# Kernel tuning notes

Measured on AMD Instinct MI355X. Metric: run time of the kernel, lower is better.

The kernel has to match this reference:

```python
import jax, jax.numpy as jnp
import numpy as np

P_THRESHOLD = 0.6
K_CAP = 16


def softmax_m1(x):
    # f(x) = (exp(x)-1) / sum(exp(x)-1), as in the torch module
    fx = jnp.expm1(x)
    return fx / fx.sum(-1, keepdims=True)


def align_chars(start_map, nb_map, max_ch):
    # eval-mode recurrence of NeighborDecoder.align_chars, run for a fixed
    # max_ch steps (no data-dependent early break; char_masks carry the
    # finished state exactly as in torch).
    b = start_map.shape[0]

    def step(carry, i):
        char_map, finished = carry  # [b, N+1], [b] int32
        mask = (finished == 0).astype(char_map.dtype)
        out = (char_map, mask)  # emitted BEFORE the update, matching torch
        finished = finished + (char_map[:, -1] > P_THRESHOLD).astype(jnp.int32)
        kk = jnp.minimum(1 + 2 * i, K_CAP).astype(char_map.dtype)
        cmd = softmax_m1(jax.lax.stop_gradient(char_map) * kk)  # .detach() in torch
        nxt = jnp.einsum('bn,bnm->bm', cmd, nb_map)
        return (nxt, finished), out

    init = (start_map, jnp.zeros(b, jnp.int32))
    _, (maps, masks) = jax.lax.scan(step, init, jnp.arange(max_ch))
    return maps.transpose(1, 0, 2), masks.T  # [b, T, N+1], [b, T]


def setup_inputs() -> dict:
    key = jax.random.key(0)
    ks = jax.random.split(key, 8)
    b, c, h, w = 32, 384, 16, 64
    num_classes = 97
    s = 1.0 / np.sqrt(c)
    return {
        'x': jax.random.normal(ks[0], (b, c, h, w), jnp.float32),
        'eos_emb': (jax.random.normal(ks[1], (c,), jnp.float32) * 0.02),
        'q_w': jax.random.normal(ks[2], (c, c), jnp.float32) * s,
        'q_b': jnp.zeros((c,), jnp.float32),
        'k_w': jax.random.normal(ks[3], (c, c), jnp.float32) * s,
        'k_b': jnp.zeros((c,), jnp.float32),
        'nav_w': jax.random.normal(ks[4], (1, c, c), jnp.float32) * 0.01,
        'nav_b': jnp.zeros((1,), jnp.float32),
        'cls_w': jax.random.normal(ks[5], (num_classes, c), jnp.float32) * s,
        'cls_b': jnp.zeros((num_classes,), jnp.float32),
        'max_char': 48,
    }


def reference(x, eos_emb, q_w, q_b, k_w, k_b, nav_w, nav_b, cls_w, cls_b, max_char):
    b, c, h, w = x.shape
    scale = float(c) ** 0.5
    xt = x.reshape(b, c, h * w).transpose(0, 2, 1)  # [b, N, c]
    g = xt.mean(axis=1)  # [b, c]
    x_ext = jnp.concatenate(
        [xt, jnp.broadcast_to(eos_emb, (b, 1, c))], axis=1)  # [b, N+1, c]

    q_start = g @ q_w.T + q_b                      # [b, c]
    k_feat = x_ext @ k_w.T + k_b                   # [b, N+1, c]
    start_map = jnp.einsum('bnc,bc->bn', k_feat, q_start) / scale
    start_map = jax.nn.softmax(start_map, axis=1)  # [b, N+1]

    q_feat = xt @ q_w.T + q_b                      # [b, N, c]
    # BilinearLayer with out=1: einsum('bim,mn,bjn->bij') + bias
    nb_map = jnp.einsum('bim,mn,bjn->bij', q_feat, nav_w[0], k_feat) + nav_b[0]
    nb_map = jax.nn.softmax(nb_map / scale, axis=2)  # [b, N, N+1]

    last = jnp.zeros((h * w + 1,), x.dtype).at[-1].set(1.0)
    nb_map = jnp.concatenate(
        [nb_map, jnp.broadcast_to(last, (b, 1, h * w + 1))], axis=1)  # [b, N+1, N+1]

    char_maps, char_masks = align_chars(start_map, nb_map, max_char)
    char_feats = jnp.einsum('btn,bnc->btc', char_maps, x_ext)
    char_feats = char_feats * char_masks[..., None]
    logits = char_feats @ cls_w.T + cls_b          # [b, T, num_classes]
    return logits, char_feats, char_maps, char_masks, nb_map
```

## Files before the change

### kernel.cpp

```cpp
#include <hip/hip_runtime.h>
#include <cstdint>
#include <cstddef>

#define BB   32
#define CC   384
#define NN   1024
#define N1   1025
#define TT   48
#define NCLS 97
#define NBL_LD 1088
#define NBTS   1056

static constexpr float INV_SCALE = 1.0f / 19.595917942265423f;

using bf16x8 = __attribute__((ext_vector_type(8))) __bf16;
using f32x4  = __attribute__((ext_vector_type(4))) float;

static constexpr size_t OFF_LOGITS = 0;
static constexpr size_t OFF_CFEAT  = 148992;
static constexpr size_t OFF_CMAPS  = 738816;
static constexpr size_t OFF_CMASK  = 2313216;
static constexpr size_t OFF_NB     = 2314752;

static constexpr size_t OFF_XB     = 0;
static constexpr size_t OFF_WGEM   = 25165824;
static constexpr size_t OFF_BIAS   = 25755648;
static constexpr size_t OFF_G      = 25758720;
static constexpr size_t OFF_QSTART = 25807872;
static constexpr size_t OFF_KEOS   = 25857024;
static constexpr size_t OFF_STATS  = 25858560;
static constexpr size_t OFF_MAPSBF = 26120704;
static constexpr size_t OFF_CMD    = 29266432;
static constexpr size_t OFF_PSUM   = 29536768;
static constexpr size_t OFF_XBT    = 29569536;
static constexpr size_t OFF_NBL    = 29569536;
static constexpr size_t OFF_OUT    = 100942336;
static constexpr size_t OFF_NBT    = 100942336;

__device__ __forceinline__ float bf2f(uint u) {
    union { uint i; float f; } v; v.i = u << 16; return v.f;
}
__device__ __forceinline__ ushort f2bf(float f) {
    union { float f; uint i; } v; v.f = f;
    uint r = v.i + 0x7fffu + ((v.i >> 16) & 1u);
    return (ushort)(r >> 16);
}

__global__ __launch_bounds__(256) void k_conv_mean(
    const float* __restrict__ x, ushort* __restrict__ xb, float* __restrict__ g)
{
    int row  = blockIdx.x * 4 + (threadIdx.x >> 6);
    int lane = threadIdx.x & 63;
    const float* src = x + (size_t)row * NN;
    ushort* dst = xb + (size_t)row * NN;
    float s = 0.f;
#pragma unroll
    for (int q = 0; q < 4; q++) {
        float4 v = ((const float4*)src)[q * 64 + lane];
        s += v.x + v.y + v.z + v.w;
        ushort4 p; p.x = f2bf(v.x); p.y = f2bf(v.y); p.z = f2bf(v.z); p.w = f2bf(v.w);
        ((ushort4*)dst)[q * 64 + lane] = p;
    }
#pragma unroll
    for (int o = 32; o; o >>= 1) s += __shfl_down(s, o);
    if (lane == 0) g[row] = s * (1.0f / NN);
}

__global__ __launch_bounds__(256) void k_transpose(
    const ushort* __restrict__ xb, ushort* __restrict__ xbT)
{
    int b = blockIdx.z, c0 = blockIdx.x * 64, n0 = blockIdx.y * 64;
    __shared__ ushort t[64][65];
    int ur = threadIdx.x >> 5, uc = threadIdx.x & 31;
    const ushort* src = xb + ((size_t)b * CC + c0) * NN + n0;
#pragma unroll
    for (int p = 0; p < 8; p++) {
        int c = p * 8 + ur;
        uint v = ((const uint*)(src + (size_t)c * NN))[uc];
        t[c][uc * 2]     = (ushort)(v & 0xffffu);
        t[c][uc * 2 + 1] = (ushort)(v >> 16);
    }
    __syncthreads();
    ushort* dst = xbT + ((size_t)b * N1 + n0) * CC + c0;
#pragma unroll
    for (int p = 0; p < 8; p++) {
        int n = p * 8 + ur;
        uint v = (uint)t[uc * 2][n] | (((uint)t[uc * 2 + 1][n]) << 16);
        ((uint*)(dst + (size_t)n * CC))[uc] = v;
    }
}

__global__ void k_eosrow(const float* __restrict__ eos, ushort* __restrict__ xbT)
{
    int c = threadIdx.x;
    xbT[((size_t)blockIdx.x * N1 + NN) * CC + c] = f2bf(eos[c]);
}

__global__ void k_wk(const float* __restrict__ k_w, const float* __restrict__ k_b,
                     ushort* __restrict__ Wgem, float* __restrict__ bias)
{
    int j = blockIdx.x, c = threadIdx.x;
    Wgem[(size_t)j * CC + c] = f2bf(k_w[(size_t)j * CC + c]);
    if (c == 0) bias[j] = k_b[j];
}

__global__ void k_w2(const float* __restrict__ nav_w, const float* __restrict__ q_w,
                     const float* __restrict__ q_b, ushort* __restrict__ Wgem,
                     float* __restrict__ bias)
{
    int m = blockIdx.x, c = threadIdx.x;
    float acc = 0.f, accb = 0.f;
    for (int k = 0; k < CC; k++) {
        float nv = nav_w[(size_t)k * CC + m];
        acc  += nv * q_w[(size_t)k * CC + c];
        accb += nv * q_b[k];
    }
    Wgem[(size_t)(CC + m) * CC + c] = f2bf(acc);
    if (c == 0) bias[CC + m] = accb;
}

__global__ void k_qstart(const float* __restrict__ g, const float* __restrict__ q_w,
                         const float* __restrict__ q_b, float* __restrict__ q_start)
{
    int b = blockIdx.x, k = threadIdx.x;
    __shared__ float gs[CC];
    gs[k] = g[(size_t)b * CC + k];
    __syncthreads();
    float acc = q_b[k];
    const float* w = q_w + (size_t)k * CC;
    for (int c = 0; c < CC; c++) acc += gs[c] * w[c];
    q_start[(size_t)b * CC + k] = acc;
}

__global__ void k_keos(const float* __restrict__ eos, const float* __restrict__ k_w,
                       const float* __restrict__ k_b, float* __restrict__ keos,
                       ushort* __restrict__ Out)
{
    int co = threadIdx.x;
    float acc = k_b[co];
    const float* w = k_w + (size_t)co * CC;
    for (int c = 0; c < CC; c++) acc += eos[c] * w[c];
    keos[co] = acc;
    ushort v = f2bf(acc);
    for (int b = 0; b < BB; b++) Out[((size_t)b * N1 + NN) * 768 + co] = v;
}

template<int MODE, int NTN, int PERB>
__global__ __launch_bounds__(256) void k_gemm(
    const ushort* __restrict__ Aall, size_t strideAb, int lda,
    const ushort* __restrict__ Ball, size_t strideBb, int ldb,
    ushort* __restrict__ Cout, size_t strideCb, int ldc,
    const float* __restrict__ bias)
{
    int wid = blockIdx.x;
    int xcd = wid & 7;
    int work = xcd * (PERB * 4) + (wid >> 3);
    int b = work / PERB;
    int r = work - b * PERB;
    int m0 = (r / NTN) * 128, n0 = (r % NTN) * 128;

    const ushort* A  = Aall + (size_t)b * strideAb;
    const ushort* Bp = Ball + (size_t)b * strideBb;
    __shared__ ushort sbuf[16384];
    ushort* As = sbuf;
    ushort* Bs = sbuf + 8192;
    int tid = threadIdx.x, wave = tid >> 6, lane = tid & 63;
    int wm = wave >> 1, wn = wave & 1;
    f32x4 acc[4][4] = {};

    uint4 ra[4], rb[4];
    auto load_tiles = [&](int k0) {
#pragma unroll
        for (int q = 0; q < 4; q++) {
            int idx = q * 256 + tid, rr = idx >> 3, c8 = (idx & 7) * 8;
            ra[q] = *(const uint4*)(A  + (size_t)(m0 + rr) * lda + k0 + c8);
            rb[q] = *(const uint4*)(Bp + (size_t)(n0 + rr) * ldb + k0 + c8);
        }
    };
    load_tiles(0);
    for (int k0 = 0; k0 < CC; k0 += 64) {
        __syncthreads();
#pragma unroll
        for (int q = 0; q < 4; q++) {
            int idx = q * 256 + tid, rr = idx >> 3, c8 = (idx & 7) * 8;
            *(uint4*)(As + rr * 64 + c8) = ra[q];
            *(uint4*)(Bs + rr * 64 + c8) = rb[q];
        }
        __syncthreads();
        if (k0 + 64 < CC) load_tiles(k0 + 64);
#pragma unroll
        for (int h = 0; h < 2; h++) {
            bf16x8 af[4], bfr[4];
#pragma unroll
            for (int i = 0; i < 4; i++) {
                int row = wm * 64 + i * 16 + (lane & 15);
                af[i]  = *(const bf16x8*)(As + row * 64 + h * 32 + (lane >> 4) * 8);
                int col = wn * 64 + i * 16 + (lane & 15);
                bfr[i] = *(const bf16x8*)(Bs + col * 64 + h * 32 + (lane >> 4) * 8);
            }
#pragma unroll
            for (int i = 0; i < 4; i++)
#pragma unroll
                for (int j = 0; j < 4; j++)
                    acc[i][j] = __builtin_amdgcn_mfma_f32_16x16x32_bf16(af[i], bfr[j], acc[i][j], 0, 0, 0);
        }
    }
    __syncthreads();
#pragma unroll
    for (int i = 0; i < 4; i++) {
        int rl = wm * 64 + i * 16 + ((lane >> 4) << 2);
#pragma unroll
        for (int j = 0; j < 4; j++) {
            int cl = wn * 64 + j * 16 + (lane & 15);
            float bv = (MODE == 0) ? bias[n0 + cl] : 0.f;
#pragma unroll
            for (int rr = 0; rr < 4; rr++) {
                float val = (MODE == 0) ? (acc[i][j][rr] + bv) : (acc[i][j][rr] * INV_SCALE);
                sbuf[(rl + rr) * 128 + cl] = f2bf(val);
            }
        }
    }
    __syncthreads();
    ushort* Cb = Cout + (size_t)b * strideCb;
#pragma unroll
    for (int q = 0; q < 8; q++) {
        int idx = q * 256 + tid, row = idx >> 4, seg = idx & 15;
        *(uint4*)(Cb + (size_t)(m0 + row) * ldc + n0 + seg * 8) =
            *(const uint4*)(sbuf + row * 128 + seg * 8);
    }
}

__global__ __launch_bounds__(1024) void k_start(
    const ushort* __restrict__ Out, const float* __restrict__ q_start,
    float* __restrict__ cmaps)
{
    int b = blockIdx.x, tid = threadIdx.x;
    __shared__ float qs[CC];
    __shared__ float red[16];
    __shared__ float bc;
    if (tid < CC) qs[tid] = q_start[(size_t)b * CC + tid];
    __syncthreads();
    auto dot = [&](int n) {
        const uint4* row = (const uint4*)(Out + ((size_t)b * N1 + n) * 768);
        float acc = 0.f;
        for (int c8 = 0; c8 < CC / 8; c8++) {
            uint4 u = row[c8];
            const ushort* us = (const ushort*)&u;
#pragma unroll
            for (int e = 0; e < 8; e++) acc += bf2f(us[e]) * qs[c8 * 8 + e];
        }
        return acc * INV_SCALE;
    };
    float v0 = dot(tid);
    float v1 = (tid == 0) ? dot(1024) : -1e30f;
    float lm = fmaxf(v0, v1);
#pragma unroll
    for (int o = 32; o; o >>= 1) lm = fmaxf(lm, __shfl_down(lm, o));
    if ((tid & 63) == 0) red[tid >> 6] = lm;
    __syncthreads();
    if (tid == 0) { float m = red[0]; for (int i = 1; i < 16; i++) m = fmaxf(m, red[i]); bc = m; }
    __syncthreads();
    float bmax = bc;
    float e0 = __expf(v0 - bmax);
    float e1 = (tid == 0) ? __expf(v1 - bmax) : 0.f;
    float ls = e0 + e1;
#pragma unroll
    for (int o = 32; o; o >>= 1) ls += __shfl_down(ls, o);
    if ((tid & 63) == 0) red[tid >> 6] = ls;
    __syncthreads();
    if (tid == 0) { float s = 0.f; for (int i = 0; i < 16; i++) s += red[i]; bc = s; }
    __syncthreads();
    float inv = 1.f / bc;
    float* o = cmaps + ((size_t)b * TT) * N1;
    o[tid] = e0 * inv;
    if (tid == 0) o[1024] = e1 * inv;
}

__global__ __launch_bounds__(256) void k_eoscol_nbl(
    const ushort* __restrict__ Out, const float* __restrict__ keos, ushort* __restrict__ nbL)
{
    int gw = blockIdx.x * 4 + (threadIdx.x >> 6);
    int lane = threadIdx.x & 63;
    for (int rr = 0; rr < 4; rr++) {
        int gi = gw * 4 + rr, b = gi >> 10, i = gi & 1023;
        const ushort* row = Out + ((size_t)b * N1 + i) * 768 + 384;
        float acc = 0.f;
        for (int c = lane; c < CC; c += 64) acc += bf2f(row[c]) * keos[c];
#pragma unroll
        for (int o = 32; o; o >>= 1) acc += __shfl_down(acc, o);
        if (lane == 0) nbL[((size_t)b * N1 + i) * NBL_LD + 1024] = f2bf(acc * INV_SCALE);
    }
}

__global__ __launch_bounds__(256) void k_softnb2(
    const ushort* __restrict__ nbL, float* __restrict__ nb, float2* __restrict__ stats)
{
    int bi = blockIdx.x;
    int b = bi >> 10, i = bi & 1023;
    const ushort* row = nbL + ((size_t)b * N1 + i) * NBL_LD;
    int tid = threadIdx.x;
    uint2 u = *(const uint2*)(row + tid * 4);
    float v0 = bf2f(u.x & 0xffffu), v1 = bf2f(u.x >> 16);
    float v2 = bf2f(u.y & 0xffffu), v3 = bf2f(u.y >> 16);
    float vt = (tid == 0) ? bf2f(row[1024]) : -1e30f;
    __shared__ float r1[4]; __shared__ float bc;
    float lm = fmaxf(fmaxf(fmaxf(v0, v1), fmaxf(v2, v3)), vt);
#pragma unroll
    for (int o = 32; o; o >>= 1) lm = fmaxf(lm, __shfl_down(lm, o));
    if ((tid & 63) == 0) r1[tid >> 6] = lm;
    __syncthreads();
    if (tid == 0) bc = fmaxf(fmaxf(r1[0], r1[1]), fmaxf(r1[2], r1[3]));
    __syncthreads();
    float m = bc;
    float e0 = __expf(v0 - m), e1 = __expf(v1 - m), e2 = __expf(v2 - m), e3 = __expf(v3 - m);
    float et = (tid == 0) ? __expf(vt - m) : 0.f;
    float s = e0 + e1 + e2 + e3 + et;
#pragma unroll
    for (int o = 32; o; o >>= 1) s += __shfl_down(s, o);
    if ((tid & 63) == 0) r1[tid >> 6] = s;
    __syncthreads();
    if (tid == 0) bc = r1[0] + r1[1] + r1[2] + r1[3];
    __syncthreads();
    float inv = 1.f / bc;
    float* orow = nb + ((size_t)b * N1 + i) * N1;
    orow[tid * 4 + 0] = e0 * inv;
    orow[tid * 4 + 1] = e1 * inv;
    orow[tid * 4 + 2] = e2 * inv;
    orow[tid * 4 + 3] = e3 * inv;
    if (tid == 0) { orow[1024] = et * inv; stats[b * 1024 + i] = make_float2(m, inv); }
}

__global__ void k_onehot2(float* __restrict__ nb, ushort* __restrict__ nbT)
{
    int b = blockIdx.x;
    float* row = nb + ((size_t)b * N1 + NN) * N1;
    for (int j = threadIdx.x; j < N1; j += 256) {
        row[j] = (j == 1024) ? 1.f : 0.f;
        nbT[((size_t)b * N1 + j) * NBTS + 1024] = (j == 1024) ? (ushort)0x3F80 : (ushort)0;
    }
}

__global__ __launch_bounds__(256) void k_transq(
    const ushort* __restrict__ nbL, const float2* __restrict__ stats,
    ushort* __restrict__ nbT)
{
    int b = blockIdx.z, n0 = blockIdx.x * 64, j0 = blockIdx.y * 64;
    __shared__ ushort tile[64][80];
    __shared__ float2 st[64];
    int tid = threadIdx.x;
    if (tid < 64) st[tid] = stats[b * 1024 + n0 + tid];
    __syncthreads();
#pragma unroll
    for (int q = 0; q < 2; q++) {
        int idx = q * 256 + tid, rl = idx >> 3, ch = idx & 7;
        const ushort* src = nbL + ((size_t)b * N1 + n0 + rl) * NBL_LD + j0 + ch * 8;
        uint4 u = *(const uint4*)src;
        float2 s = st[rl];
        const ushort* us = (const ushort*)&u;
#pragma unroll
        for (int k = 0; k < 8; k++)
            tile[ch * 8 + k][rl] = f2bf(__expf(bf2f(us[k]) - s.x) * s.y);
    }
    __syncthreads();
#pragma unroll
    for (int q = 0; q < 2; q++) {
        int idx = q * 256 + tid, jl = idx >> 3, seg = idx & 7;
        int j = j0 + jl;
        if (j <= 1024) {
            uint4 v = *(const uint4*)&tile[jl][seg * 8];
            *(uint4*)(nbT + ((size_t)b * N1 + j) * NBTS + n0 + seg * 8) = v;
        }
    }
}

__global__ __launch_bounds__(256) void k_cmd0(
    const float* __restrict__ cmaps, float* __restrict__ cmd_out, float* __restrict__ ps_out)
{
    int b = blockIdx.x, tid = threadIdx.x;
    __shared__ float red[4];
    const float* m = cmaps + (size_t)b * TT * N1;
    float s = 0.f;
    for (int n = tid; n < N1; n += 256) {
        float c = expm1f(m[n]);
        cmd_out[(size_t)b * 1056 + n] = c;
        s += c;
    }
#pragma unroll
    for (int o = 32; o; o >>= 1) s += __shfl_down(s, o);
    if ((tid & 63) == 0) red[tid >> 6] = s;
    __syncthreads();
    if (tid == 0) ps_out[b * 128] = red[0] + red[1] + red[2] + red[3];
    else if (tid < 128) ps_out[b * 128 + tid] = 0.f;
}

__global__ __launch_bounds__(256) void k_step2(
    float* __restrict__ cmaps, const ushort* __restrict__ nbT,
    const float* __restrict__ cmd_in, float* __restrict__ cmd_out,
    const float* __restrict__ ps_in, float* __restrict__ ps_out, int t)
{
    int b = blockIdx.y, blk = blockIdx.x, j0 = blk * 16;
    int tid = threadIdx.x, wave = tid >> 6, lane = tid & 63;
    const ushort* base = nbT + (size_t)b * N1 * NBTS;
    uint4 rv[4][2]; ushort tl[4];
#pragma unroll
    for (int r = 0; r < 4; r++) {
        int j = j0 + wave * 4 + r; if (j > 1024) j = 1024;
        const ushort* row = base + (size_t)j * NBTS;
        rv[r][0] = *(const uint4*)(row + lane * 8);
        rv[r][1] = *(const uint4*)(row + 512 + lane * 8);
        tl[r] = row[1024];
    }
    __shared__ __align__(16) float cmd[1028];
    __shared__ float red[8];
    const float* ci = cmd_in + (size_t)b * 1056;
    *(float4*)(cmd + tid * 4) = *(const float4*)(ci + tid * 4);
    if (tid == 0) cmd[1024] = ci[1024];
    float pv = (tid < 65) ? ps_in[b * 128 + tid] : 0.f;
#pragma unroll
    for (int o = 32; o; o >>= 1) pv += __shfl_down(pv, o);
    if (lane == 0) red[wave] = pv;
    __syncthreads();
    float inv = 1.f / (red[0] + red[1] + red[2] + red[3]);
    int kkn = 3 + 2 * t; if (kkn > 16) kkn = 16;
    float kknf = (float)kkn;
    float cns = 0.f;
#pragma unroll
    for (int r = 0; r < 4; r++) {
        const ushort* p0 = (const ushort*)&rv[r][0];
        const ushort* p1 = (const ushort*)&rv[r][1];
        int n0 = lane * 8;
        float acc = 0.f;
#pragma unroll
        for (int e = 0; e < 8; e++) acc += bf2f(p0[e]) * cmd[n0 + e];
#pragma unroll
        for (int e = 0; e < 8; e++) acc += bf2f(p1[e]) * cmd[512 + n0 + e];
#pragma unroll
        for (int o = 32; o; o >>= 1) acc += __shfl_down(acc, o);
        int j = j0 + wave * 4 + r;
        if (lane == 0 && j <= 1024) {
            acc += cmd[1024] * bf2f(tl[r]);
            float mo = acc * inv;
            cmaps[((size_t)b * TT + t + 1) * N1 + j] = mo;
            float cn = expm1f(kknf * mo);
            cmd_out[(size_t)b * 1056 + j] = cn;
            cns += cn;
        }
    }
    if (lane == 0) red[4 + wave] = cns;
    __syncthreads();
    if (tid == 0) ps_out[b * 128 + blk] = red[4] + red[5] + red[6] + red[7];
}

__global__ void k_masks(const float* __restrict__ cmaps, float* __restrict__ cmask)
{
    int b = threadIdx.x;
    if (b < BB) {
        int fin = 0;
        for (int t = 0; t < TT; t++) {
            cmask[b * TT + t] = (fin == 0) ? 1.f : 0.f;
            fin += (cmaps[((size_t)b * TT + t) * N1 + 1024] > 0.6f) ? 1 : 0;
        }
    }
}

__global__ void k_mapsbf(const float* __restrict__ cmaps, ushort* __restrict__ mb)
{
    size_t i = (size_t)blockIdx.x * 256 + threadIdx.x;
    size_t bt = i >> 10; int n = (int)(i & 1023);
    mb[i] = f2bf(cmaps[bt * N1 + n]);
}

__global__ __launch_bounds__(256) void k_cfeat(
    const ushort* __restrict__ mapsbf, const ushort* __restrict__ xb,
    const float* __restrict__ cmaps, const float* __restrict__ eos,
    const float* __restrict__ masks, float* __restrict__ cfeat)
{
    int b = blockIdx.x;
    int wave = threadIdx.x >> 6, lane = threadIdx.x & 63;
    f32x4 acc[3][6] = {};
    const ushort* Ab = mapsbf + (size_t)b * TT * 1024;
    const ushort* Bb = xb + (size_t)b * CC * NN;
    for (int k0 = 0; k0 < NN; k0 += 32) {
        int kk_ = k0 + (lane >> 4) * 8;
        bf16x8 af[3], bfr[6];
#pragma unroll
        for (int i = 0; i < 3; i++)
            af[i] = *(const bf16x8*)(Ab + (size_t)(i * 16 + (lane & 15)) * 1024 + kk_);
#pragma unroll
        for (int j = 0; j < 6; j++)
            bfr[j] = *(const bf16x8*)(Bb + (size_t)(wave * 96 + j * 16 + (lane & 15)) * NN + kk_);
#pragma unroll
        for (int i = 0; i < 3; i++)
#pragma unroll
            for (int j = 0; j < 6; j++)
                acc[i][j] = __builtin_amdgcn_mfma_f32_16x16x32_bf16(af[i], bfr[j], acc[i][j], 0, 0, 0);
    }
#pragma unroll
    for (int i = 0; i < 3; i++) {
        int tbase = i * 16 + ((lane >> 4) << 2);
#pragma unroll
        for (int j = 0; j < 6; j++) {
            int c = wave * 96 + j * 16 + (lane & 15);
            float ev = eos[c];
#pragma unroll
            for (int rr = 0; rr < 4; rr++) {
                int tt = tbase + rr;
                float mlast = cmaps[((size_t)b * TT + tt) * N1 + 1024];
                float val = (acc[i][j][rr] + mlast * ev) * masks[b * TT + tt];
                cfeat[((size_t)b * TT + tt) * CC + c] = val;
            }
        }
    }
}

__global__ __launch_bounds__(128) void k_logits(
    const float* __restrict__ cfeat, const float* __restrict__ cls_w,
    const float* __restrict__ cls_b, float* __restrict__ out)
{
    int bt = blockIdx.x;
    __shared__ float row[CC];
    for (int c = threadIdx.x; c < CC; c += 128) row[c] = cfeat[(size_t)bt * CC + c];
    __syncthreads();
    int j = threadIdx.x;
    if (j < NCLS) {
        float acc = cls_b[j];
        const float* w = cls_w + (size_t)j * CC;
        for (int c = 0; c < CC; c++) acc += row[c] * w[c];
        out[(size_t)bt * NCLS + j] = acc;
    }
}

extern "C" void kernel_launch(void* const* d_in, const int* in_sizes, int n_in,
                              void* d_out, int out_size, void* d_ws, size_t ws_size,
                              hipStream_t stream)
{
    (void)in_sizes; (void)n_in; (void)out_size; (void)ws_size;
    const float* x     = (const float*)d_in[0];
    const float* eos   = (const float*)d_in[1];
    const float* q_w   = (const float*)d_in[2];
    const float* q_b   = (const float*)d_in[3];
    const float* k_w   = (const float*)d_in[4];
    const float* k_b   = (const float*)d_in[5];
    const float* nav_w = (const float*)d_in[6];
    const float* cls_w = (const float*)d_in[8];
    const float* cls_b = (const float*)d_in[9];

    char* ws = (char*)d_ws;
    ushort* xb     = (ushort*)(ws + OFF_XB);
    ushort* Wgem   = (ushort*)(ws + OFF_WGEM);
    float*  bias   = (float*)(ws + OFF_BIAS);
    float*  g      = (float*)(ws + OFF_G);
    float*  qstart = (float*)(ws + OFF_QSTART);
    float*  keos   = (float*)(ws + OFF_KEOS);
    float2* stats  = (float2*)(ws + OFF_STATS);
    ushort* mapsbf = (ushort*)(ws + OFF_MAPSBF);
    float*  cmdbuf = (float*)(ws + OFF_CMD);
    float*  psbuf  = (float*)(ws + OFF_PSUM);
    ushort* xbT    = (ushort*)(ws + OFF_XBT);
    ushort* nbL    = (ushort*)(ws + OFF_NBL);
    ushort* Out    = (ushort*)(ws + OFF_OUT);
    ushort* nbT    = (ushort*)(ws + OFF_NBT);

    float* out     = (float*)d_out;
    float* logits  = out + OFF_LOGITS;
    float* cfeat   = out + OFF_CFEAT;
    float* cmaps   = out + OFF_CMAPS;
    float* cmask   = out + OFF_CMASK;
    float* nb      = out + OFF_NB;

    k_conv_mean<<<3072, 256, 0, stream>>>(x, xb, g);
    k_transpose<<<dim3(6, 16, BB), 256, 0, stream>>>(xb, xbT);
    k_eosrow<<<BB, CC, 0, stream>>>(eos, xbT);
    k_wk<<<CC, CC, 0, stream>>>(k_w, k_b, Wgem, bias);
    k_w2<<<CC, CC, 0, stream>>>(nav_w, q_w, q_b, Wgem, bias);
    k_qstart<<<BB, CC, 0, stream>>>(g, q_w, q_b, qstart);
    k_keos<<<1, CC, 0, stream>>>(eos, k_w, k_b, keos, Out);

    k_gemm<0, 6, 48><<<1536, 256, 0, stream>>>(
        xbT, (size_t)N1 * CC, CC, Wgem, 0, CC, Out, (size_t)N1 * 768, 768, bias);

    k_start<<<BB, 1024, 0, stream>>>(Out, qstart, cmaps);
    k_cmd0<<<BB, 256, 0, stream>>>(cmaps, cmdbuf, psbuf);
    k_eoscol_nbl<<<2048, 256, 0, stream>>>(Out, keos, nbL);

    k_gemm<1, 8, 64><<<2048, 256, 0, stream>>>(
        Out + 384, (size_t)N1 * 768, 768, Out, (size_t)N1 * 768, 768,
        nbL, (size_t)N1 * NBL_LD, NBL_LD, nullptr);

    k_softnb2<<<BB * NN, 256, 0, stream>>>(nbL, nb, stats);
    k_onehot2<<<BB, 256, 0, stream>>>(nb, nbT);
    k_transq<<<dim3(16, 17, BB), 256, 0, stream>>>(nbL, stats, nbT);

    for (int t = 0; t < TT - 1; t++)
        k_step2<<<dim3(65, BB), 256, 0, stream>>>(
            cmaps, nbT,
            cmdbuf + (size_t)(t & 1) * 33792, cmdbuf + (size_t)((t + 1) & 1) * 33792,
            psbuf + (size_t)(t & 1) * 4096,  psbuf + (size_t)((t + 1) & 1) * 4096, t);

    k_masks<<<1, 64, 0, stream>>>(cmaps, cmask);
    k_mapsbf<<<6144, 256, 0, stream>>>(cmaps, mapsbf);
    k_cfeat<<<BB, 256, 0, stream>>>(mapsbf, xb, cmaps, eos, cmask, cfeat);
    k_logits<<<BB * TT, 128, 0, stream>>>(cfeat, cls_w, cls_b, logits);
}
```

Measured before the change: 1.165 ms.

## Fuse recurrence steps into one persistent kernel with per-batch spin barriers

Replaces the 47 per-step recurrence launches with a single persistent kernel of 256 blocks, eight per batch, that loops over all steps. Blocks sync through an atomic counter per batch and exchange char maps through global memory. Each block recomputes the expm1 and softmax normaliser itself, and row loads are double-buffered. The change also XOR-swizzles the GEMM shared-memory tiles to avoid bank conflicts and vectorises the softmax row store; the risks are spin-barrier deadlock if blocks are not all co-resident, and the extra redundant expm1 work per block.

```diff
diff --git a/kernel.cpp b/kernel.cpp
--- a/kernel.cpp
+++ b/kernel.cpp
@@ -30,8 +30,7 @@
 static constexpr size_t OFF_KEOS   = 25857024;
 static constexpr size_t OFF_STATS  = 25858560;
 static constexpr size_t OFF_MAPSBF = 26120704;
-static constexpr size_t OFF_CMD    = 29266432;
-static constexpr size_t OFF_PSUM   = 29536768;
+static constexpr size_t OFF_BAR    = 29266432;
 static constexpr size_t OFF_XBT    = 29569536;
 static constexpr size_t OFF_NBL    = 29569536;
 static constexpr size_t OFF_OUT    = 100942336;
@@ -182,21 +181,23 @@
         __syncthreads();
 #pragma unroll
         for (int q = 0; q < 4; q++) {
-            int idx = q * 256 + tid, rr = idx >> 3, c8 = (idx & 7) * 8;
-            *(uint4*)(As + rr * 64 + c8) = ra[q];
-            *(uint4*)(Bs + rr * 64 + c8) = rb[q];
+            int idx = q * 256 + tid, rr = idx >> 3, ch = idx & 7;
+            int sw = (ch ^ (rr & 7)) << 3;
+            *(uint4*)(As + rr * 64 + sw) = ra[q];
+            *(uint4*)(Bs + rr * 64 + sw) = rb[q];
         }
         __syncthreads();
         if (k0 + 64 < CC) load_tiles(k0 + 64);
 #pragma unroll
         for (int h = 0; h < 2; h++) {
             bf16x8 af[4], bfr[4];
+            int chb = h * 4 + (lane >> 4);
 #pragma unroll
             for (int i = 0; i < 4; i++) {
                 int row = wm * 64 + i * 16 + (lane & 15);
-                af[i]  = *(const bf16x8*)(As + row * 64 + h * 32 + (lane >> 4) * 8);
+                af[i]  = *(const bf16x8*)(As + row * 64 + ((chb ^ (row & 7)) << 3));
                 int col = wn * 64 + i * 16 + (lane & 15);
-                bfr[i] = *(const bf16x8*)(Bs + col * 64 + h * 32 + (lane >> 4) * 8);
+                bfr[i] = *(const bf16x8*)(Bs + col * 64 + ((chb ^ (col & 7)) << 3));
             }
 #pragma unroll
             for (int i = 0; i < 4; i++)
@@ -323,21 +324,17 @@
     __syncthreads();
     float inv = 1.f / bc;
     float* orow = nb + ((size_t)b * N1 + i) * N1;
-    orow[tid * 4 + 0] = e0 * inv;
-    orow[tid * 4 + 1] = e1 * inv;
-    orow[tid * 4 + 2] = e2 * inv;
-    orow[tid * 4 + 3] = e3 * inv;
+    float4 ov = make_float4(e0 * inv, e1 * inv, e2 * inv, e3 * inv);
+    *(float4*)(orow + tid * 4) = ov;
     if (tid == 0) { orow[1024] = et * inv; stats[b * 1024 + i] = make_float2(m, inv); }
 }
 
-__global__ void k_onehot2(float* __restrict__ nb, ushort* __restrict__ nbT)
+__global__ void k_onehot(float* __restrict__ nb)
 {
     int b = blockIdx.x;
     float* row = nb + ((size_t)b * N1 + NN) * N1;
-    for (int j = threadIdx.x; j < N1; j += 256) {
+    for (int j = threadIdx.x; j < N1; j += 256)
         row[j] = (j == 1024) ? 1.f : 0.f;
-        nbT[((size_t)b * N1 + j) * NBTS + 1024] = (j == 1024) ? (ushort)0x3F80 : (ushort)0;
-    }
 }
 
 __global__ __launch_bounds__(256) void k_transq(
@@ -373,82 +370,120 @@
     }
 }
 
-__global__ __launch_bounds__(256) void k_cmd0(
-    const float* __restrict__ cmaps, float* __restrict__ cmd_out, float* __restrict__ ps_out)
-{
-    int b = blockIdx.x, tid = threadIdx.x;
-    __shared__ float red[4];
-    const float* m = cmaps + (size_t)b * TT * N1;
-    float s = 0.f;
-    for (int n = tid; n < N1; n += 256) {
-        float c = expm1f(m[n]);
-        cmd_out[(size_t)b * 1056 + n] = c;
-        s += c;
-    }
-#pragma unroll
-    for (int o = 32; o; o >>= 1) s += __shfl_down(s, o);
-    if ((tid & 63) == 0) red[tid >> 6] = s;
-    __syncthreads();
-    if (tid == 0) ps_out[b * 128] = red[0] + red[1] + red[2] + red[3];
-    else if (tid < 128) ps_out[b * 128 + tid] = 0.f;
-}
-
-__global__ __launch_bounds__(256) void k_step2(
-    float* __restrict__ cmaps, const ushort* __restrict__ nbT,
-    const float* __restrict__ cmd_in, float* __restrict__ cmd_out,
-    const float* __restrict__ ps_in, float* __restrict__ ps_out, int t)
-{
-    int b = blockIdx.y, blk = blockIdx.x, j0 = blk * 16;
+__global__ void k_barinit(uint* __restrict__ bar) { bar[threadIdx.x] = 0u; }
+
+__device__ __forceinline__ float dot16(uint4 r0, uint4 r1,
+                                       const float* cA, const float* cB)
+{
+    const ushort* p0 = (const ushort*)&r0;
+    const ushort* p1 = (const ushort*)&r1;
+    float acc = 0.f;
+#pragma unroll
+    for (int e = 0; e < 8; e++) acc += bf2f(p0[e]) * cA[e];
+#pragma unroll
+    for (int e = 0; e < 8; e++) acc += bf2f(p1[e]) * cB[e];
+    return acc;
+}
+
+__global__ __launch_bounds__(512) void k_rec(
+    float* __restrict__ cmaps, const ushort* __restrict__ nbT, uint* __restrict__ bar)
+{
+    int blk = blockIdx.x;
+    int b = blk >> 3, chunk = blk & 7;
     int tid = threadIdx.x, wave = tid >> 6, lane = tid & 63;
+    int j0 = chunk * 128;
     const ushort* base = nbT + (size_t)b * N1 * NBTS;
-    uint4 rv[4][2]; ushort tl[4];
-#pragma unroll
-    for (int r = 0; r < 4; r++) {
-        int j = j0 + wave * 4 + r; if (j > 1024) j = 1024;
-        const ushort* row = base + (size_t)j * NBTS;
-        rv[r][0] = *(const uint4*)(row + lane * 8);
-        rv[r][1] = *(const uint4*)(row + 512 + lane * 8);
-        tl[r] = row[1024];
-    }
     __shared__ __align__(16) float cmd[1028];
     __shared__ float red[8];
-    const float* ci = cmd_in + (size_t)b * 1056;
-    *(float4*)(cmd + tid * 4) = *(const float4*)(ci + tid * 4);
-    if (tid == 0) cmd[1024] = ci[1024];
-    float pv = (tid < 65) ? ps_in[b * 128 + tid] : 0.f;
-#pragma unroll
-    for (int o = 32; o; o >>= 1) pv += __shfl_down(pv, o);
-    if (lane == 0) red[wave] = pv;
-    __syncthreads();
-    float inv = 1.f / (red[0] + red[1] + red[2] + red[3]);
-    int kkn = 3 + 2 * t; if (kkn > 16) kkn = 16;
-    float kknf = (float)kkn;
-    float cns = 0.f;
-#pragma unroll
-    for (int r = 0; r < 4; r++) {
-        const ushort* p0 = (const ushort*)&rv[r][0];
-        const ushort* p1 = (const ushort*)&rv[r][1];
-        int n0 = lane * 8;
-        float acc = 0.f;
-#pragma unroll
-        for (int e = 0; e < 8; e++) acc += bf2f(p0[e]) * cmd[n0 + e];
-#pragma unroll
-        for (int e = 0; e < 8; e++) acc += bf2f(p1[e]) * cmd[512 + n0 + e];
-#pragma unroll
-        for (int o = 32; o; o >>= 1) acc += __shfl_down(acc, o);
-        int j = j0 + wave * 4 + r;
-        if (lane == 0 && j <= 1024) {
-            acc += cmd[1024] * bf2f(tl[r]);
-            float mo = acc * inv;
-            cmaps[((size_t)b * TT + t + 1) * N1 + j] = mo;
-            float cn = expm1f(kknf * mo);
-            cmd_out[(size_t)b * 1056 + j] = cn;
-            cns += cn;
-        }
-    }
-    if (lane == 0) red[4 + wave] = cns;
-    __syncthreads();
-    if (tid == 0) ps_out[b * 128 + blk] = red[4] + red[5] + red[6] + red[7];
+    __shared__ float sinv;
+
+    for (int t = 0; t < TT - 1; ++t) {
+        const float* mrow = cmaps + ((size_t)b * TT + t) * N1;
+        int kki = 1 + 2 * t; if (kki > 16) kki = 16;
+        float kkf = (float)kki;
+        float part = 0.f;
+#pragma unroll
+        for (int q = 0; q < 2; ++q) {
+            int n = q * 512 + tid;
+            float m = __hip_atomic_load(mrow + n, __ATOMIC_RELAXED, __HIP_MEMORY_SCOPE_AGENT);
+            float e = expm1f(kkf * m);
+            cmd[n] = e; part += e;
+        }
+        if (tid == 0) {
+            float m = __hip_atomic_load(mrow + 1024, __ATOMIC_RELAXED, __HIP_MEMORY_SCOPE_AGENT);
+            float e = expm1f(kkf * m);
+            cmd[1024] = e; part += e;
+        }
+#pragma unroll
+        for (int o = 32; o; o >>= 1) part += __shfl_down(part, o);
+        if (lane == 0) red[wave] = part;
+        __syncthreads();
+        if (tid == 0) {
+            float s = 0.f;
+#pragma unroll
+            for (int w = 0; w < 8; w++) s += red[w];
+            sinv = 1.f / s;
+        }
+        __syncthreads();
+        float inv = sinv;
+        float cA[8], cB[8];
+        *(float4*)&cA[0] = *(const float4*)(cmd + lane * 8);
+        *(float4*)&cA[4] = *(const float4*)(cmd + lane * 8 + 4);
+        *(float4*)&cB[0] = *(const float4*)(cmd + 512 + lane * 8);
+        *(float4*)&cB[4] = *(const float4*)(cmd + 512 + lane * 8 + 4);
+        float* orow = cmaps + ((size_t)b * TT + t + 1) * N1;
+        int rbase = j0 + wave * 16;
+
+        uint4 cur[4][2], nxt[4][2];
+#pragma unroll
+        for (int r = 0; r < 4; ++r) {
+            const ushort* row = base + (size_t)(rbase + r) * NBTS;
+            cur[r][0] = *(const uint4*)(row + lane * 8);
+            cur[r][1] = *(const uint4*)(row + 512 + lane * 8);
+        }
+        for (int g = 0; g < 4; ++g) {
+            if (g < 3) {
+#pragma unroll
+                for (int r = 0; r < 4; ++r) {
+                    const ushort* row = base + (size_t)(rbase + (g + 1) * 4 + r) * NBTS;
+                    nxt[r][0] = *(const uint4*)(row + lane * 8);
+                    nxt[r][1] = *(const uint4*)(row + 512 + lane * 8);
+                }
+            }
+#pragma unroll
+            for (int r = 0; r < 4; ++r) {
+                float acc = dot16(cur[r][0], cur[r][1], cA, cB);
+#pragma unroll
+                for (int o = 32; o; o >>= 1) acc += __shfl_down(acc, o);
+                if (lane == 0)
+                    __hip_atomic_store(orow + rbase + g * 4 + r, acc * inv,
+                                       __ATOMIC_RELAXED, __HIP_MEMORY_SCOPE_AGENT);
+            }
+            if (g < 3) {
+#pragma unroll
+                for (int r = 0; r < 4; ++r) { cur[r][0] = nxt[r][0]; cur[r][1] = nxt[r][1]; }
+            }
+        }
+        if (chunk == 7 && wave == 7) {
+            const ushort* row = base + (size_t)1024 * NBTS;
+            uint4 r0 = *(const uint4*)(row + lane * 8);
+            uint4 r1 = *(const uint4*)(row + 512 + lane * 8);
+            float acc = dot16(r0, r1, cA, cB);
+#pragma unroll
+            for (int o = 32; o; o >>= 1) acc += __shfl_down(acc, o);
+            if (lane == 0)
+                __hip_atomic_store(orow + 1024, (acc + cmd[1024]) * inv,
+                                   __ATOMIC_RELAXED, __HIP_MEMORY_SCOPE_AGENT);
+        }
+        __syncthreads();
+        if (tid == 0) {
+            __hip_atomic_fetch_add(&bar[b], 1u, __ATOMIC_RELEASE, __HIP_MEMORY_SCOPE_AGENT);
+            uint want = 8u * (uint)(t + 1);
+            while (__hip_atomic_load(&bar[b], __ATOMIC_ACQUIRE, __HIP_MEMORY_SCOPE_AGENT) < want)
+                __builtin_amdgcn_s_sleep(8);
+        }
+        __syncthreads();
+    }
 }
 
 __global__ void k_masks(const float* __restrict__ cmaps, float* __restrict__ cmask)
@@ -554,8 +589,7 @@
     float*  keos   = (float*)(ws + OFF_KEOS);
     float2* stats  = (float2*)(ws + OFF_STATS);
     ushort* mapsbf = (ushort*)(ws + OFF_MAPSBF);
-    float*  cmdbuf = (float*)(ws + OFF_CMD);
-    float*  psbuf  = (float*)(ws + OFF_PSUM);
+    uint*   bar    = (uint*)(ws + OFF_BAR);
     ushort* xbT    = (ushort*)(ws + OFF_XBT);
     ushort* nbL    = (ushort*)(ws + OFF_NBL);
     ushort* Out    = (ushort*)(ws + OFF_OUT);
@@ -575,12 +609,12 @@
     k_w2<<<CC, CC, 0, stream>>>(nav_w, q_w, q_b, Wgem, bias);
     k_qstart<<<BB, CC, 0, stream>>>(g, q_w, q_b, qstart);
     k_keos<<<1, CC, 0, stream>>>(eos, k_w, k_b, keos, Out);
+    k_barinit<<<1, 32, 0, stream>>>(bar);
 
     k_gemm<0, 6, 48><<<1536, 256, 0, stream>>>(
         xbT, (size_t)N1 * CC, CC, Wgem, 0, CC, Out, (size_t)N1 * 768, 768, bias);
 
     k_start<<<BB, 1024, 0, stream>>>(Out, qstart, cmaps);
-    k_cmd0<<<BB, 256, 0, stream>>>(cmaps, cmdbuf, psbuf);
     k_eoscol_nbl<<<2048, 256, 0, stream>>>(Out, keos, nbL);
 
     k_gemm<1, 8, 64><<<2048, 256, 0, stream>>>(
@@ -588,14 +622,10 @@
         nbL, (size_t)N1 * NBL_LD, NBL_LD, nullptr);
 
     k_softnb2<<<BB * NN, 256, 0, stream>>>(nbL, nb, stats);
-    k_onehot2<<<BB, 256, 0, stream>>>(nb, nbT);
+    k_onehot<<<BB, 256, 0, stream>>>(nb);
     k_transq<<<dim3(16, 17, BB), 256, 0, stream>>>(nbL, stats, nbT);
 
-    for (int t = 0; t < TT - 1; t++)
-        k_step2<<<dim3(65, BB), 256, 0, stream>>>(
-            cmaps, nbT,
-            cmdbuf + (size_t)(t & 1) * 33792, cmdbuf + (size_t)((t + 1) & 1) * 33792,
-            psbuf + (size_t)(t & 1) * 4096,  psbuf + (size_t)((t + 1) & 1) * 4096, t);
+    k_rec<<<256, 512, 0, stream>>>(cmaps, nbT, bar);
 
     k_masks<<<1, 64, 0, stream>>>(cmaps, cmask);
     k_mapsbf<<<6144, 256, 0, stream>>>(cmaps, mapsbf);
```

New measurement: 1.925 ms (median of 5 runs). 65.3% more time.

## Swizzle GEMM LDS tiles, restructure recurrence step to row-per-lane with fewer blocks

Applied to the files above, without the earlier changes.

The GEMM's shared-memory tiles get an XOR swizzle on the 8-element chunk index to reduce LDS bank conflicts on the MFMA fragment reads. The per-step recurrence kernel now gives each lane one output row and each wave a quarter of the reduction dimension. It runs 17 blocks per batch instead of 65, with a software-prefetched register pipeline, and drops the cross-lane shuffle reductions per row. The nbT eos column is no longer written, and the eos term is added only for row 1024. The softmax output store is vectorised to float4. The new step layout has each lane reading a separate row, so memory accesses are strided across lanes and may coalesce worse.

```diff
diff --git a/kernel.cpp b/kernel.cpp
--- a/kernel.cpp
+++ b/kernel.cpp
@@ -182,21 +182,23 @@
         __syncthreads();
 #pragma unroll
         for (int q = 0; q < 4; q++) {
-            int idx = q * 256 + tid, rr = idx >> 3, c8 = (idx & 7) * 8;
-            *(uint4*)(As + rr * 64 + c8) = ra[q];
-            *(uint4*)(Bs + rr * 64 + c8) = rb[q];
+            int idx = q * 256 + tid, rr = idx >> 3, ch = idx & 7;
+            int sw = (ch ^ (rr & 7)) << 3;
+            *(uint4*)(As + rr * 64 + sw) = ra[q];
+            *(uint4*)(Bs + rr * 64 + sw) = rb[q];
         }
         __syncthreads();
         if (k0 + 64 < CC) load_tiles(k0 + 64);
 #pragma unroll
         for (int h = 0; h < 2; h++) {
             bf16x8 af[4], bfr[4];
+            int chb = h * 4 + (lane >> 4);
 #pragma unroll
             for (int i = 0; i < 4; i++) {
                 int row = wm * 64 + i * 16 + (lane & 15);
-                af[i]  = *(const bf16x8*)(As + row * 64 + h * 32 + (lane >> 4) * 8);
+                af[i]  = *(const bf16x8*)(As + row * 64 + ((chb ^ (row & 7)) << 3));
                 int col = wn * 64 + i * 16 + (lane & 15);
-                bfr[i] = *(const bf16x8*)(Bs + col * 64 + h * 32 + (lane >> 4) * 8);
+                bfr[i] = *(const bf16x8*)(Bs + col * 64 + ((chb ^ (col & 7)) << 3));
             }
 #pragma unroll
             for (int i = 0; i < 4; i++)
@@ -323,21 +325,17 @@
     __syncthreads();
     float inv = 1.f / bc;
     float* orow = nb + ((size_t)b * N1 + i) * N1;
-    orow[tid * 4 + 0] = e0 * inv;
-    orow[tid * 4 + 1] = e1 * inv;
-    orow[tid * 4 + 2] = e2 * inv;
-    orow[tid * 4 + 3] = e3 * inv;
+    float4 ov = make_float4(e0 * inv, e1 * inv, e2 * inv, e3 * inv);
+    *(float4*)(orow + tid * 4) = ov;
     if (tid == 0) { orow[1024] = et * inv; stats[b * 1024 + i] = make_float2(m, inv); }
 }
 
-__global__ void k_onehot2(float* __restrict__ nb, ushort* __restrict__ nbT)
+__global__ void k_onehot(float* __restrict__ nb)
 {
     int b = blockIdx.x;
     float* row = nb + ((size_t)b * N1 + NN) * N1;
-    for (int j = threadIdx.x; j < N1; j += 256) {
+    for (int j = threadIdx.x; j < N1; j += 256)
         row[j] = (j == 1024) ? 1.f : 0.f;
-        nbT[((size_t)b * N1 + j) * NBTS + 1024] = (j == 1024) ? (ushort)0x3F80 : (ushort)0;
-    }
 }
 
 __global__ __launch_bounds__(256) void k_transq(
@@ -393,62 +391,76 @@
     else if (tid < 128) ps_out[b * 128 + tid] = 0.f;
 }
 
-__global__ __launch_bounds__(256) void k_step2(
+__global__ __launch_bounds__(256) void k_step3(
     float* __restrict__ cmaps, const ushort* __restrict__ nbT,
     const float* __restrict__ cmd_in, float* __restrict__ cmd_out,
     const float* __restrict__ ps_in, float* __restrict__ ps_out, int t)
 {
-    int b = blockIdx.y, blk = blockIdx.x, j0 = blk * 16;
+    int b = blockIdx.y, blk = blockIdx.x;
     int tid = threadIdx.x, wave = tid >> 6, lane = tid & 63;
-    const ushort* base = nbT + (size_t)b * N1 * NBTS;
-    uint4 rv[4][2]; ushort tl[4];
-#pragma unroll
-    for (int r = 0; r < 4; r++) {
-        int j = j0 + wave * 4 + r; if (j > 1024) j = 1024;
-        const ushort* row = base + (size_t)j * NBTS;
-        rv[r][0] = *(const uint4*)(row + lane * 8);
-        rv[r][1] = *(const uint4*)(row + 512 + lane * 8);
-        tl[r] = row[1024];
-    }
+    int j0 = blk * 64;
+    int rowc = j0 + lane; if (rowc > 1024) rowc = 1024;
+    const ushort* rp = nbT + ((size_t)b * N1 + rowc) * NBTS + wave * 256;
+
+    uint4 buf[8];
+#pragma unroll
+    for (int p = 0; p < 8; ++p) buf[p] = *(const uint4*)(rp + p * 8);
+
     __shared__ __align__(16) float cmd[1028];
-    __shared__ float red[8];
+    __shared__ float partial[4][64];
+    __shared__ float sred;
     const float* ci = cmd_in + (size_t)b * 1056;
     *(float4*)(cmd + tid * 4) = *(const float4*)(ci + tid * 4);
     if (tid == 0) cmd[1024] = ci[1024];
-    float pv = (tid < 65) ? ps_in[b * 128 + tid] : 0.f;
-#pragma unroll
-    for (int o = 32; o; o >>= 1) pv += __shfl_down(pv, o);
-    if (lane == 0) red[wave] = pv;
-    __syncthreads();
-    float inv = 1.f / (red[0] + red[1] + red[2] + red[3]);
-    int kkn = 3 + 2 * t; if (kkn > 16) kkn = 16;
-    float kknf = (float)kkn;
-    float cns = 0.f;
-#pragma unroll
-    for (int r = 0; r < 4; r++) {
-        const ushort* p0 = (const ushort*)&rv[r][0];
-        const ushort* p1 = (const ushort*)&rv[r][1];
-        int n0 = lane * 8;
-        float acc = 0.f;
-#pragma unroll
-        for (int e = 0; e < 8; e++) acc += bf2f(p0[e]) * cmd[n0 + e];
-#pragma unroll
-        for (int e = 0; e < 8; e++) acc += bf2f(p1[e]) * cmd[512 + n0 + e];
-#pragma unroll
-        for (int o = 32; o; o >>= 1) acc += __shfl_down(acc, o);
-        int j = j0 + wave * 4 + r;
-        if (lane == 0 && j <= 1024) {
-            acc += cmd[1024] * bf2f(tl[r]);
-            float mo = acc * inv;
+    if (wave == 0) {
+        float pv = (lane < 17) ? ps_in[b * 128 + lane] : 0.f;
+#pragma unroll
+        for (int o = 16; o; o >>= 1) pv += __shfl_down(pv, o);
+        if (lane == 0) sred = pv;
+    }
+    __syncthreads();
+    float inv = 1.f / sred;
+
+    const float* cq = cmd + wave * 256;
+    float acc = 0.f;
+    for (int g = 0; g < 4; ++g) {
+        uint4 nbuf[8];
+        if (g < 3) {
+#pragma unroll
+            for (int p = 0; p < 8; ++p)
+                nbuf[p] = *(const uint4*)(rp + (g + 1) * 64 + p * 8);
+        }
+#pragma unroll
+        for (int p = 0; p < 8; ++p) {
+            const ushort* u = (const ushort*)&buf[p];
+            const float* cc = cq + g * 64 + p * 8;
+#pragma unroll
+            for (int e = 0; e < 8; ++e) acc += bf2f(u[e]) * cc[e];
+        }
+        if (g < 3) {
+#pragma unroll
+            for (int p = 0; p < 8; ++p) buf[p] = nbuf[p];
+        }
+    }
+    partial[wave][lane] = acc;
+    __syncthreads();
+    if (wave == 0) {
+        int j = j0 + lane;
+        bool valid = (j <= 1024);
+        float s = partial[0][lane] + partial[1][lane] + partial[2][lane] + partial[3][lane];
+        if (j == 1024) s += cmd[1024];
+        float mo = s * inv;
+        int kkn = 3 + 2 * t; if (kkn > 16) kkn = 16;
+        float cn = valid ? expm1f((float)kkn * mo) : 0.f;
+        if (valid) {
             cmaps[((size_t)b * TT + t + 1) * N1 + j] = mo;
-            float cn = expm1f(kknf * mo);
             cmd_out[(size_t)b * 1056 + j] = cn;
-            cns += cn;
-        }
-    }
-    if (lane == 0) red[4 + wave] = cns;
-    __syncthreads();
-    if (tid == 0) ps_out[b * 128 + blk] = red[4] + red[5] + red[6] + red[7];
+        }
+        float ps = cn;
+#pragma unroll
+        for (int o = 32; o; o >>= 1) ps += __shfl_down(ps, o);
+        if (lane == 0) ps_out[b * 128 + blk] = ps;
+    }
 }
 
 __global__ void k_masks(const float* __restrict__ cmaps, float* __restrict__ cmask)
@@ -588,11 +600,11 @@
         nbL, (size_t)N1 * NBL_LD, NBL_LD, nullptr);
 
     k_softnb2<<<BB * NN, 256, 0, stream>>>(nbL, nb, stats);
-    k_onehot2<<<BB, 256, 0, stream>>>(nb, nbT);
+    k_onehot<<<BB, 256, 0, stream>>>(nb);
     k_transq<<<dim3(16, 17, BB), 256, 0, stream>>>(nbL, stats, nbT);
 
     for (int t = 0; t < TT - 1; t++)
-        k_step2<<<dim3(65, BB), 256, 0, stream>>>(
+        k_step3<<<dim3(17, BB), 256, 0, stream>>>(
             cmaps, nbT,
             cmdbuf + (size_t)(t & 1) * 33792, cmdbuf + (size_t)((t + 1) & 1) * 33792,
             psbuf + (size_t)(t & 1) * 4096,  psbuf + (size_t)((t + 1) & 1) * 4096, t);
```

Result: slower. 1.399 ms (+20.2%).
